# Optimization experiments

Measured on AMD Instinct MI355X. Metric: run time of the kernel, lower is better.

The kernel has to match this reference:

```python
import jax, jax.numpy as jnp
import numpy as np

EPS = 1e-6


def _forward(x, weight_compress, weight_expand, body_w1, body_b1, body_w2, body_b2,
             route_w, route_b, off_w, off_b, out_h, out_w):
    b, C, h, w = x.shape
    E, r, _ = weight_compress.shape
    scale_h = out_h / h
    scale_w = out_w / w

    # --- scale-aware coordinate features: [out_h, out_w, 4] ---
    ch = (jnp.arange(out_h, dtype=jnp.float32) + 0.5) / scale_h
    coor_h = ch - jnp.floor(ch + EPS) - 0.5            # [H]
    cw = (jnp.arange(out_w, dtype=jnp.float32) + 0.5) / scale_w
    coor_w = cw - jnp.floor(cw + EPS) - 0.5            # [W]
    ones = jnp.ones((out_h, out_w), jnp.float32)
    feat = jnp.stack([ones / scale_w, ones / scale_h,
                      coor_h[:, None] * ones, coor_w[None, :] * ones], axis=-1)

    # --- body (1x1 convs == per-pixel MLP), routing, offset ---
    emb = jax.nn.gelu(feat @ body_w1.T + body_b1, approximate=False)
    emb = jax.nn.gelu(emb @ body_w2.T + body_b2, approximate=False)   # [H,W,64]
    routing = jax.nn.sigmoid(emb @ route_w.T + route_b)               # [H,W,E]
    offset = emb @ off_w.T + off_b                                    # [H,W,2]

    # --- per-pixel soft-MoE weight mixing ---
    rw = routing.reshape(-1, E)                                       # [HW,E]
    wc = (rw @ weight_compress.reshape(E, -1)).reshape(out_h, out_w, r, C)
    we = (rw @ weight_expand.reshape(E, -1)).reshape(out_h, out_w, C, r)

    # --- grid_sample with learned offsets (bilinear, zero padding, align_corners=False) ---
    gx = ((jnp.arange(out_w, dtype=jnp.float32) + 0.5) / scale_w - 0.5) * 2.0 / (w - 1) - 1.0
    gy = ((jnp.arange(out_h, dtype=jnp.float32) + 0.5) / scale_h - 0.5) * 2.0 / (h - 1) - 1.0
    gx2 = gx[None, :] + offset[..., 0] * 2.0 / (w - 1)                # [H,W]
    gy2 = gy[:, None] + offset[..., 1] * 2.0 / (h - 1)                # [H,W]
    ix = (gx2 + 1.0) * w / 2.0 - 0.5
    iy = (gy2 + 1.0) * h / 2.0 - 0.5
    x0 = jnp.floor(ix); x1 = x0 + 1.0
    y0 = jnp.floor(iy); y1 = y0 + 1.0
    wx1 = ix - x0; wx0 = 1.0 - wx1
    wy1 = iy - y0; wy0 = 1.0 - wy1

    def gather(yy, xx):
        valid = ((xx >= 0) & (xx <= w - 1) & (yy >= 0) & (yy <= h - 1)).astype(x.dtype)
        xi = jnp.clip(xx, 0, w - 1).astype(jnp.int32)
        yi = jnp.clip(yy, 0, h - 1).astype(jnp.int32)
        return x[:, :, yi, xi] * valid[None, None]                    # [B,C,H,W]

    fea0 = (gather(y0, x0) * (wy0 * wx0)[None, None]
            + gather(y0, x1) * (wy0 * wx1)[None, None]
            + gather(y1, x0) * (wy1 * wx0)[None, None]
            + gather(y1, x1) * (wy1 * wx1)[None, None])               # [B,C,H,W]

    # --- per-pixel dynamic compress/expand matmuls ---
    mid = jnp.einsum('hwrc,bchw->bhwr', wc, fea0)
    out = jnp.einsum('hwcr,bhwr->bchw', we, mid)
    return out + fea0


def setup_inputs() -> dict:
    key = jax.random.key(0)
    ks = jax.random.split(key, 12)
    C, E, r, hid = 64, 4, 4, 64
    s = 0.1
    return {
        'x': jax.random.normal(ks[0], (4, C, 192, 192), jnp.float32),
        'weight_compress': jax.random.normal(ks[1], (E, r, C), jnp.float32) * s,
        'weight_expand': jax.random.normal(ks[2], (E, C, r), jnp.float32) * s,
        'body_w1': jax.random.normal(ks[3], (hid, 4), jnp.float32) * 0.5,
        'body_b1': jax.random.normal(ks[4], (hid,), jnp.float32) * 0.1,
        'body_w2': jax.random.normal(ks[5], (hid, hid), jnp.float32) * (1.0 / np.sqrt(hid)),
        'body_b2': jax.random.normal(ks[6], (hid,), jnp.float32) * 0.1,
        'route_w': jax.random.normal(ks[7], (E, hid), jnp.float32) * (1.0 / np.sqrt(hid)),
        'route_b': jax.random.normal(ks[8], (E,), jnp.float32) * 0.1,
        'off_w': jax.random.normal(ks[9], (2, hid), jnp.float32) * (1.0 / np.sqrt(hid)),
        'off_b': jax.random.normal(ks[10], (2,), jnp.float32) * 0.1,
        'out_h': 384,
        'out_w': 384,
    }


def reference(x, weight_compress, weight_expand, body_w1, body_b1, body_w2, body_b2,
              route_w, route_b, off_w, off_b, out_h, out_w):
    return _forward(x, weight_compress, weight_expand, body_w1, body_b1, body_w2,
                    body_b2, route_w, route_b, off_w, off_b, out_h, out_w)
```

## Files before the change

### kernel.cpp

```cpp
#include <hip/hip_runtime.h>
#include <math.h>

#define BB 4
#define CC 64
#define IH 192
#define IW 192
#define OH 384
#define OW 384
#define NE 4
#define NR 4
#define HID 64

__device__ __forceinline__ float gelu_exact(float v) {
    return 0.5f * v * (1.0f + erff(v * 0.70710678118654752f));
}

__global__ void precompute_kernel(
    const float* __restrict__ wcomp, const float* __restrict__ wexp,
    const float* __restrict__ bw1, const float* __restrict__ bb1,
    const float* __restrict__ bw2, const float* __restrict__ bb2,
    const float* __restrict__ rw, const float* __restrict__ rb,
    const float* __restrict__ ow, const float* __restrict__ ob,
    float* __restrict__ ws)
{
    __shared__ float s_e1[4][HID];
    __shared__ float s_e2[4][HID];
    __shared__ float s_rt[4][NE];
    const int tid = threadIdx.x;
    const int p = tid >> 6;
    const int j = tid & 63;
    const float ch = (p & 2) ? 0.25f : -0.25f;
    const float cw = (p & 1) ? 0.25f : -0.25f;
    float a = bw1[j*4+0]*0.5f + bw1[j*4+1]*0.5f + bw1[j*4+2]*ch + bw1[j*4+3]*cw + bb1[j];
    s_e1[p][j] = gelu_exact(a);
    __syncthreads();
    float acc = bb2[j];
    #pragma unroll 8
    for (int k = 0; k < HID; ++k) acc += bw2[j*HID+k]*s_e1[p][k];
    s_e2[p][j] = gelu_exact(acc);
    __syncthreads();
    if (j < NE) {
        float s = rb[j];
        for (int k = 0; k < HID; ++k) s += rw[j*HID+k]*s_e2[p][k];
        s_rt[p][j] = 1.0f/(1.0f+expf(-s));
    } else if (j < NE+2) {
        const int d = j - NE;
        float s = ob[d];
        for (int k = 0; k < HID; ++k) s += ow[d*HID+k]*s_e2[p][k];
        ws[2048 + p*2 + d] = s;
    }
    __syncthreads();
    const int c = j;
    const float r0 = s_rt[p][0], r1 = s_rt[p][1], r2 = s_rt[p][2], r3 = s_rt[p][3];
    #pragma unroll
    for (int r = 0; r < NR; ++r) {
        float v = r0*wcomp[0*NR*CC + r*CC + c] + r1*wcomp[1*NR*CC + r*CC + c]
                + r2*wcomp[2*NR*CC + r*CC + c] + r3*wcomp[3*NR*CC + r*CC + c];
        ws[(p*CC + c)*4 + r] = v;
        float u = r0*wexp[0*CC*NR + c*NR + r] + r1*wexp[1*CC*NR + c*NR + r]
                + r2*wexp[2*CC*NR + c*NR + r] + r3*wexp[3*CC*NR + c*NR + r];
        ws[1024 + (p*CC + c)*4 + r] = u;
    }
}

__global__ __launch_bounds__(256, 4) void upsample_kernel(
    const float* __restrict__ x, const float* __restrict__ ws,
    float* __restrict__ out)
{
    __shared__ __align__(16) float s_tab[2056];
    __shared__ float4 s_mid[4][64];
    const int lane = threadIdx.x;
    const int cg   = threadIdx.y;
    const int tid  = cg*64 + lane;
    for (int i = tid; i < 2056; i += 256) s_tab[i] = ws[i];
    __syncthreads();

    const int pix = blockIdx.x * 64 + lane;
    const int b   = pix / (OH*OW);
    const int rem = pix - b*(OH*OW);
    const int oy  = rem / OW;
    const int ox  = rem - oy*OW;
    const int p   = ((oy & 1) << 1) | (ox & 1);

    const float offx = s_tab[2048 + p*2 + 0];
    const float offy = s_tab[2048 + p*2 + 1];

    const float inv_w1 = 2.0f / 191.0f;
    float gx2 = (((ox + 0.5f)*0.5f - 0.5f) * inv_w1 - 1.0f) + offx * inv_w1;
    float gy2 = (((oy + 0.5f)*0.5f - 0.5f) * inv_w1 - 1.0f) + offy * inv_w1;
    float ix = (gx2 + 1.0f) * 96.0f - 0.5f;
    float iy = (gy2 + 1.0f) * 96.0f - 0.5f;

    float x0f = floorf(ix), y0f = floorf(iy);
    float wx1 = ix - x0f, wx0 = 1.0f - wx1;
    float wy1 = iy - y0f, wy0 = 1.0f - wy1;
    float x1f = x0f + 1.0f, y1f = y0f + 1.0f;
    float vx0 = (x0f >= 0.0f && x0f <= 191.0f) ? 1.0f : 0.0f;
    float vx1 = (x1f >= 0.0f && x1f <= 191.0f) ? 1.0f : 0.0f;
    float vy0 = (y0f >= 0.0f && y0f <= 191.0f) ? 1.0f : 0.0f;
    float vy1 = (y1f >= 0.0f && y1f <= 191.0f) ? 1.0f : 0.0f;
    const float w00 = wy0*wx0*vy0*vx0;
    const float w01 = wy0*wx1*vy0*vx1;
    const float w10 = wy1*wx0*vy1*vx0;
    const float w11 = wy1*wx1*vy1*vx1;

    const int xi0 = (int)fminf(fmaxf(x0f, 0.0f), 191.0f);
    const int xi1 = (int)fminf(fmaxf(x1f, 0.0f), 191.0f);
    const int yi0 = (int)fminf(fmaxf(y0f, 0.0f), 191.0f);
    const int yi1 = (int)fminf(fmaxf(y1f, 0.0f), 191.0f);

    const int o00 = yi0*IW + xi0;
    const int o01 = yi0*IW + xi1;
    const int o10 = yi1*IW + xi0;
    const int o11 = yi1*IW + xi1;

    const float* __restrict__ xb = x + b*(CC*IH*IW) + cg*(16*IH*IW);
    const float4* wc4 = ((const float4*)s_tab) + p*CC + cg*16;
    const float4* we4 = ((const float4*)s_tab) + 256 + p*CC + cg*16;

    float f[16];
    float4 mid = make_float4(0.f, 0.f, 0.f, 0.f);
    #pragma unroll
    for (int j = 0; j < 16; ++j) {
        const int o = j*(IH*IW);
        float v = w00*xb[o+o00] + w01*xb[o+o01] + w10*xb[o+o10] + w11*xb[o+o11];
        f[j] = v;
        float4 wc = wc4[j];
        mid.x += wc.x*v; mid.y += wc.y*v; mid.z += wc.z*v; mid.w += wc.w*v;
    }
    s_mid[cg][lane] = mid;
    __syncthreads();
    float4 m0 = s_mid[0][lane], m1 = s_mid[1][lane],
           m2 = s_mid[2][lane], m3 = s_mid[3][lane];
    const float mid0 = m0.x + m1.x + m2.x + m3.x;
    const float mid1 = m0.y + m1.y + m2.y + m3.y;
    const float mid2 = m0.z + m1.z + m2.z + m3.z;
    const float mid3 = m0.w + m1.w + m2.w + m3.w;

    float* __restrict__ op = out + b*(CC*OH*OW) + cg*(16*OH*OW) + oy*OW + ox;
    #pragma unroll
    for (int j = 0; j < 16; ++j) {
        float4 we = we4[j];
        float v = f[j] + we.x*mid0 + we.y*mid1 + we.z*mid2 + we.w*mid3;
        __builtin_nontemporal_store(v, op + j*(OH*OW));
    }
}

extern "C" void kernel_launch(void* const* d_in, const int* in_sizes, int n_in,
                              void* d_out, int out_size, void* d_ws, size_t ws_size,
                              hipStream_t stream) {
    const float* x     = (const float*)d_in[0];
    const float* wcomp = (const float*)d_in[1];
    const float* wexp  = (const float*)d_in[2];
    const float* bw1   = (const float*)d_in[3];
    const float* bb1   = (const float*)d_in[4];
    const float* bw2   = (const float*)d_in[5];
    const float* bb2   = (const float*)d_in[6];
    const float* rw    = (const float*)d_in[7];
    const float* rb    = (const float*)d_in[8];
    const float* ow    = (const float*)d_in[9];
    const float* ob    = (const float*)d_in[10];
    float* ws  = (float*)d_ws;
    float* out = (float*)d_out;

    precompute_kernel<<<1, 256, 0, stream>>>(wcomp, wexp, bw1, bb1, bw2, bb2,
                                             rw, rb, ow, ob, ws);
    const int total_pix = BB*OH*OW;
    dim3 block(64, 4);
    upsample_kernel<<<total_pix/64, block, 0, stream>>>(x, ws, out);
}
```

Before: 243.5 us.

## Compute two output rows per thread sharing input row loads

Each thread now handles two output pixels two rows apart with the same phase. They share a middle input row, so six gathers per channel replace eight, and the grid becomes a 3D layout over column tiles, row pairs and batch. The pixel ordering also changes: lanes interleave even and odd columns, and the sampling math is simplified algebraically. Nontemporal stores become ordinary stores and the occupancy hint in the launch bounds is removed, which may raise register pressure from holding 32 outputs per thread.

After: 236.8 us. 2.7% less time.

```diff
diff --git a/kernel.cpp b/kernel.cpp
--- a/kernel.cpp
+++ b/kernel.cpp
@@ -63,86 +63,102 @@
     }
 }
 
-__global__ __launch_bounds__(256, 4) void upsample_kernel(
+__global__ __launch_bounds__(256) void upsample_kernel(
     const float* __restrict__ x, const float* __restrict__ ws,
     float* __restrict__ out)
 {
     __shared__ __align__(16) float s_tab[2056];
-    __shared__ float4 s_mid[4][64];
+    __shared__ float4 s_mid[4][2][64];
     const int lane = threadIdx.x;
     const int cg   = threadIdx.y;
     const int tid  = cg*64 + lane;
     for (int i = tid; i < 2056; i += 256) s_tab[i] = ws[i];
     __syncthreads();
 
-    const int pix = blockIdx.x * 64 + lane;
-    const int b   = pix / (OH*OW);
-    const int rem = pix - b*(OH*OW);
-    const int oy  = rem / OW;
-    const int ox  = rem - oy*OW;
-    const int p   = ((oy & 1) << 1) | (ox & 1);
+    const int half = lane >> 5;
+    const int i32  = lane & 31;
+    const int ox   = blockIdx.x*64 + 2*i32 + half;
+    const int rp   = blockIdx.y;
+    const int oy_a = ((rp >> 1) << 2) + (rp & 1);
+    const int oy_b = oy_a + 2;
+    const int b    = blockIdx.z;
+    const int p    = ((rp & 1) << 1) | half;
 
     const float offx = s_tab[2048 + p*2 + 0];
     const float offy = s_tab[2048 + p*2 + 1];
 
-    const float inv_w1 = 2.0f / 191.0f;
-    float gx2 = (((ox + 0.5f)*0.5f - 0.5f) * inv_w1 - 1.0f) + offx * inv_w1;
-    float gy2 = (((oy + 0.5f)*0.5f - 0.5f) * inv_w1 - 1.0f) + offy * inv_w1;
-    float ix = (gx2 + 1.0f) * 96.0f - 0.5f;
-    float iy = (gy2 + 1.0f) * 96.0f - 0.5f;
+    const float k191 = 192.0f / 191.0f;
+    float ix = (((ox + 0.5f)*0.5f - 0.5f) + offx) * k191 - 0.5f;
+    float iy = (((oy_a + 0.5f)*0.5f - 0.5f) + offy) * k191 - 0.5f;
 
-    float x0f = floorf(ix), y0f = floorf(iy);
-    float wx1 = ix - x0f, wx0 = 1.0f - wx1;
-    float wy1 = iy - y0f, wy0 = 1.0f - wy1;
-    float x1f = x0f + 1.0f, y1f = y0f + 1.0f;
+    float x0f = floorf(ix);
+    float wx1f = ix - x0f, wx0f = 1.0f - wx1f;
+    float x1f = x0f + 1.0f;
     float vx0 = (x0f >= 0.0f && x0f <= 191.0f) ? 1.0f : 0.0f;
     float vx1 = (x1f >= 0.0f && x1f <= 191.0f) ? 1.0f : 0.0f;
-    float vy0 = (y0f >= 0.0f && y0f <= 191.0f) ? 1.0f : 0.0f;
-    float vy1 = (y1f >= 0.0f && y1f <= 191.0f) ? 1.0f : 0.0f;
-    const float w00 = wy0*wx0*vy0*vx0;
-    const float w01 = wy0*wx1*vy0*vx1;
-    const float w10 = wy1*wx0*vy1*vx0;
-    const float w11 = wy1*wx1*vy1*vx1;
-
+    const float wx0 = wx0f * vx0;
+    const float wx1 = wx1f * vx1;
     const int xi0 = (int)fminf(fmaxf(x0f, 0.0f), 191.0f);
     const int xi1 = (int)fminf(fmaxf(x1f, 0.0f), 191.0f);
-    const int yi0 = (int)fminf(fmaxf(y0f, 0.0f), 191.0f);
-    const int yi1 = (int)fminf(fmaxf(y1f, 0.0f), 191.0f);
 
-    const int o00 = yi0*IW + xi0;
-    const int o01 = yi0*IW + xi1;
-    const int o10 = yi1*IW + xi0;
-    const int o11 = yi1*IW + xi1;
+    float y0f = floorf(iy);
+    float wy1f = iy - y0f, wy0f = 1.0f - wy1f;
+    float r0f = y0f, r1f = y0f + 1.0f, r2f = y0f + 2.0f;
+    float v0 = (r0f >= 0.0f && r0f <= 191.0f) ? 1.0f : 0.0f;
+    float v1 = (r1f >= 0.0f && r1f <= 191.0f) ? 1.0f : 0.0f;
+    float v2 = (r2f >= 0.0f && r2f <= 191.0f) ? 1.0f : 0.0f;
+    const float wya0 = wy0f * v0, wya1 = wy1f * v1;
+    const float wyb0 = wy0f * v1, wyb1 = wy1f * v2;
+    const int yi0 = (int)fminf(fmaxf(r0f, 0.0f), 191.0f);
+    const int yi1 = (int)fminf(fmaxf(r1f, 0.0f), 191.0f);
+    const int yi2 = (int)fminf(fmaxf(r2f, 0.0f), 191.0f);
+
+    const int o00 = yi0*IW + xi0, o01 = yi0*IW + xi1;
+    const int o10 = yi1*IW + xi0, o11 = yi1*IW + xi1;
+    const int o20 = yi2*IW + xi0, o21 = yi2*IW + xi1;
 
     const float* __restrict__ xb = x + b*(CC*IH*IW) + cg*(16*IH*IW);
     const float4* wc4 = ((const float4*)s_tab) + p*CC + cg*16;
     const float4* we4 = ((const float4*)s_tab) + 256 + p*CC + cg*16;
 
-    float f[16];
-    float4 mid = make_float4(0.f, 0.f, 0.f, 0.f);
+    float fa[16], fb[16];
+    float4 mida = make_float4(0.f,0.f,0.f,0.f);
+    float4 midb = make_float4(0.f,0.f,0.f,0.f);
     #pragma unroll
     for (int j = 0; j < 16; ++j) {
-        const int o = j*(IH*IW);
-        float v = w00*xb[o+o00] + w01*xb[o+o01] + w10*xb[o+o10] + w11*xb[o+o11];
-        f[j] = v;
+        const float* __restrict__ bp = xb + j*(IH*IW);
+        float a00 = bp[o00], a01 = bp[o01];
+        float a10 = bp[o10], a11 = bp[o11];
+        float a20 = bp[o20], a21 = bp[o21];
+        float rd0 = wx0*a00 + wx1*a01;
+        float rd1 = wx0*a10 + wx1*a11;
+        float rd2 = wx0*a20 + wx1*a21;
+        float va = wya0*rd0 + wya1*rd1;
+        float vb = wyb0*rd1 + wyb1*rd2;
+        fa[j] = va; fb[j] = vb;
         float4 wc = wc4[j];
-        mid.x += wc.x*v; mid.y += wc.y*v; mid.z += wc.z*v; mid.w += wc.w*v;
+        mida.x += wc.x*va; mida.y += wc.y*va; mida.z += wc.z*va; mida.w += wc.w*va;
+        midb.x += wc.x*vb; midb.y += wc.y*vb; midb.z += wc.z*vb; midb.w += wc.w*vb;
     }
-    s_mid[cg][lane] = mid;
+    s_mid[cg][0][lane] = mida;
+    s_mid[cg][1][lane] = midb;
     __syncthreads();
-    float4 m0 = s_mid[0][lane], m1 = s_mid[1][lane],
-           m2 = s_mid[2][lane], m3 = s_mid[3][lane];
-    const float mid0 = m0.x + m1.x + m2.x + m3.x;
-    const float mid1 = m0.y + m1.y + m2.y + m3.y;
-    const float mid2 = m0.z + m1.z + m2.z + m3.z;
-    const float mid3 = m0.w + m1.w + m2.w + m3.w;
+    float4 a0 = s_mid[0][0][lane], a1 = s_mid[1][0][lane],
+           a2 = s_mid[2][0][lane], a3 = s_mid[3][0][lane];
+    float4 b0 = s_mid[0][1][lane], b1 = s_mid[1][1][lane],
+           b2 = s_mid[2][1][lane], b3 = s_mid[3][1][lane];
+    const float ma0 = a0.x+a1.x+a2.x+a3.x, ma1 = a0.y+a1.y+a2.y+a3.y;
+    const float ma2 = a0.z+a1.z+a2.z+a3.z, ma3 = a0.w+a1.w+a2.w+a3.w;
+    const float mb0 = b0.x+b1.x+b2.x+b3.x, mb1 = b0.y+b1.y+b2.y+b3.y;
+    const float mb2 = b0.z+b1.z+b2.z+b3.z, mb3 = b0.w+b1.w+b2.w+b3.w;
 
-    float* __restrict__ op = out + b*(CC*OH*OW) + cg*(16*OH*OW) + oy*OW + ox;
+    float* __restrict__ opa = out + b*(CC*OH*OW) + cg*(16*OH*OW) + oy_a*OW + ox;
+    float* __restrict__ opb = opa + 2*OW;
     #pragma unroll
     for (int j = 0; j < 16; ++j) {
         float4 we = we4[j];
-        float v = f[j] + we.x*mid0 + we.y*mid1 + we.z*mid2 + we.w*mid3;
-        __builtin_nontemporal_store(v, op + j*(OH*OW));
+        opa[j*(OH*OW)] = fa[j] + we.x*ma0 + we.y*ma1 + we.z*ma2 + we.w*ma3;
+        opb[j*(OH*OW)] = fb[j] + we.x*mb0 + we.y*mb1 + we.z*mb2 + we.w*mb3;
     }
 }
 
@@ -165,7 +181,7 @@
 
     precompute_kernel<<<1, 256, 0, stream>>>(wcomp, wexp, bw1, bb1, bw2, bb2,
                                              rw, rb, ow, ob, ws);
-    const int total_pix = BB*OH*OW;
     dim3 block(64, 4);
-    upsample_kernel<<<total_pix/64, block, 0, stream>>>(x, ws, out);
+    dim3 grid(OW/64, OH/2, BB);
+    upsample_kernel<<<grid, block, 0, stream>>>(x, ws, out);
 }
```
